# Performance work log

Hardware: AMD Instinct MI355X
Metric: run time of the kernel (lower is better)

The kernel has to match this reference:

```python
import jax, jax.numpy as jnp
import numpy as np

LAMBDA = 0.0   # lambda_value
EPS = 1e-8     # eps


def setup_inputs() -> dict:
    key = jax.random.key(0)
    k1, k2 = jax.random.split(key)
    B, T, C = 512, 256, 400
    outputs = jax.random.normal(k1, (B, T, C), dtype=jnp.float32)
    labels = jax.random.randint(k2, (B,), 0, C, dtype=jnp.int64)
    return {"outputs": outputs, "labels": labels}


def reference(outputs, labels):
    # outputs: (B, T, C) logits; labels: (B,) class indices
    B, T, C = outputs.shape
    proba = jnp.maximum(jax.nn.softmax(outputs, axis=-1), EPS)          # (B,T,C)
    idx = jnp.argmax(proba, axis=1)                                      # (B,C) argmax over time
    max_probs = jnp.maximum(jnp.max(proba, axis=1), EPS)                 # (B,C)
    # parallel prefix-max over the time axis (torch.cummax dim=1)
    cum_max = jax.lax.associative_scan(jnp.maximum, proba, axis=1)       # (B,T,C)
    sum_cum_max = jnp.sum(cum_max, axis=1)                               # (B,C)
    e_x = T - sum_cum_max / max_probs                                    # (B,C) expected exit time
    i_x = e_x / T
    log_term = jnp.log(LAMBDA + (1.0 - LAMBDA) * i_x + EPS)              # (B,C)
    per_class = -jnp.log(max_probs) + log_term                           # (B,C)
    fast_loss = jnp.take_along_axis(per_class, labels[:, None], axis=1)[:, 0]  # (B,)
    fast_loss = fast_loss.mean()                                         # reduction='mean'
    return fast_loss, idx, max_probs, e_x
```

## Files before the change

### kernel.cpp

```cpp
#include <hip/hip_runtime.h>
#include <math.h>

#define B_DIM 512
#define T_DIM 256
#define C_DIM 400
#define EPSV 1e-8f
#define TT 16
#define NT (T_DIM / TT)
#define TILE_F (TT * C_DIM)


__device__ __forceinline__ void load_tile_rows(
    const float* __restrict__ xb, int tile, int w, int ln,
    float4& a0, float4& a1, float4& b0, float4& b1) {
    const float4* r0 = (const float4*)(xb + (size_t)tile * TILE_F + (size_t)(2 * w) * C_DIM);
    const float4* r1 = (const float4*)(xb + (size_t)tile * TILE_F + (size_t)(2 * w + 1) * C_DIM);
    a0 = r0[ln];
    b0 = r1[ln];
    a1 = make_float4(-INFINITY, -INFINITY, -INFINITY, -INFINITY);
    b1 = a1;
    if (ln < 36) { a1 = r0[64 + ln]; b1 = r1[64 + ln]; }
}

__device__ __forceinline__ float wave_sum_dpp(float v) {
    int t;
    t = __builtin_amdgcn_update_dpp(0, __float_as_int(v), 0x111, 0xf, 0xf, true);
    v += __int_as_float(t);
    t = __builtin_amdgcn_update_dpp(0, __float_as_int(v), 0x112, 0xf, 0xf, true);
    v += __int_as_float(t);
    t = __builtin_amdgcn_update_dpp(0, __float_as_int(v), 0x114, 0xf, 0xf, true);
    v += __int_as_float(t);
    t = __builtin_amdgcn_update_dpp(0, __float_as_int(v), 0x118, 0xf, 0xf, true);
    v += __int_as_float(t);
    t = __builtin_amdgcn_update_dpp(0, __float_as_int(v), 0x142, 0xa, 0xf, true);
    v += __int_as_float(t);
    t = __builtin_amdgcn_update_dpp(0, __float_as_int(v), 0x143, 0xc, 0xf, true);
    v += __int_as_float(t);
    return __int_as_float(__builtin_amdgcn_readlane(__float_as_int(v), 63));
}

__device__ __forceinline__ void row_softmax_store(
    float4 v0, float4 v1, float* __restrict__ rowp, int ln) {
    float e0x = __expf(v0.x), e0y = __expf(v0.y);
    float e0z = __expf(v0.z), e0w = __expf(v0.w);
    float e1x = __expf(v1.x), e1y = __expf(v1.y);
    float e1z = __expf(v1.z), e1w = __expf(v1.w);

    float s = wave_sum_dpp(((e0x + e0y) + (e0z + e0w)) +
                           ((e1x + e1y) + (e1z + e1w)));
    float rinv = 1.0f / s;
    float4* wp = (float4*)rowp;
    wp[ln] = make_float4(e0x * rinv, e0y * rinv, e0z * rinv, e0w * rinv);
    if (ln < 36)
        wp[64 + ln] = make_float4(e1x * rinv, e1y * rinv, e1z * rinv, e1w * rinv);
}

__global__ __launch_bounds__(512, 4) void fused_kernel(
    const float* __restrict__ x, const int* __restrict__ labels,
    float* __restrict__ out, double* __restrict__ pcws) {
    __shared__ __align__(16) float buf[2][TILE_F];

    const int b   = blockIdx.x;
    const int tid = threadIdx.x;
    const int w   = tid >> 6;
    const int ln  = tid & 63;
    const int c   = w * 50 + ln;
    const bool act = (ln < 50);
    const float* xb = x + (size_t)b * T_DIM * C_DIM;

    float4 ca0, ca1, cb0, cb1, na0, na1, nb0, nb1;
    load_tile_rows(xb, 0, w, ln, ca0, ca1, cb0, cb1);

    float  cur = EPSV;
    int    arg = 0;
    double scm = 0.0;

    for (int tile = 0; tile < NT; ++tile) {
        const int pb = tile & 1;
        if (tile + 1 < NT)
            load_tile_rows(xb, tile + 1, w, ln, na0, na1, nb0, nb1);

        row_softmax_store(ca0, ca1, &buf[pb][(size_t)(2 * w) * C_DIM], ln);
        row_softmax_store(cb0, cb1, &buf[pb][(size_t)(2 * w + 1) * C_DIM], ln);

        asm volatile("s_waitcnt lgkmcnt(0)" ::: "memory");
        __builtin_amdgcn_sched_barrier(0);
        __builtin_amdgcn_s_barrier();

        if (act) {
            const float* bp = &buf[pb][c];
            float scmt = 0.0f;
            #pragma unroll
            for (int t = 0; t < TT; ++t) {
                float p = bp[(size_t)t * C_DIM];
                if (p > cur) { cur = p; arg = tile * TT + t; }
                scmt += cur;
            }
            scm += (double)scmt;
        }
        ca0 = na0; ca1 = na1; cb0 = nb0; cb1 = nb1;
    }

    if (act) {
        float  maxp = cur;
        double e_x  = (double)T_DIM - scm / (double)maxp;
        if (e_x < 0.0) e_x = 0.0;
        size_t BC = (size_t)B_DIM * C_DIM;
        size_t o  = (size_t)b * C_DIM + c;
        out[1 + o]          = (float)arg;
        out[1 + BC + o]     = maxp;
        out[1 + 2 * BC + o] = (float)e_x;
        if (c == labels[b]) {
            double i_x = e_x / (double)T_DIM;
            pcws[b] = -log((double)maxp) + log(i_x + 1e-8);
        }
    }
}

__global__ __launch_bounds__(512) void loss_kernel(
    const double* __restrict__ pcws, float* __restrict__ out) {
    __shared__ double part[8];
    double pc = pcws[threadIdx.x];
    #pragma unroll
    for (int off = 32; off > 0; off >>= 1)
        pc += __shfl_xor(pc, off, 64);
    if ((threadIdx.x & 63) == 0) part[threadIdx.x >> 6] = pc;
    __syncthreads();
    if (threadIdx.x == 0) {
        double s = 0.0;
        #pragma unroll
        for (int i = 0; i < 8; ++i) s += part[i];
        out[0] = (float)(s / (double)B_DIM);
    }
}

extern "C" void kernel_launch(void* const* d_in, const int* in_sizes, int n_in,
                              void* d_out, int out_size, void* d_ws, size_t ws_size,
                              hipStream_t stream) {
    const float* x      = (const float*)d_in[0];
    const int*   labels = (const int*)d_in[1];
    float*       out    = (float*)d_out;
    double*      pcws   = (double*)d_ws;

    fused_kernel<<<B_DIM, 512, 0, stream>>>(x, labels, out, pcws);
    loss_kernel<<<1, 512, 0, stream>>>(pcws, out);
}
```

Baseline: 40.34 us.

## Pack two batch rows per 1024-thread block with ping-pong softmax/scan phases

Each block now handles two batch rows. The two 512-thread halves alternate each step: one half writes softmax rows to its shared buffer while the other half scans its buffer for running max and argmax, so exp work and LDS scan work interleave across a shared barrier. Each half now uses a single buffer instead of double buffering. Both halves still sync on every barrier, which doubles the barrier count and halves the number of blocks. The reciprocal also changes to the fast hardware rcp, which may shift precision slightly.

```diff
diff --git a/kernel.cpp b/kernel.cpp
--- a/kernel.cpp
+++ b/kernel.cpp
@@ -48,25 +48,28 @@
 
     float s = wave_sum_dpp(((e0x + e0y) + (e0z + e0w)) +
                            ((e1x + e1y) + (e1z + e1w)));
-    float rinv = 1.0f / s;
+    float rinv = __builtin_amdgcn_rcpf(s);
     float4* wp = (float4*)rowp;
     wp[ln] = make_float4(e0x * rinv, e0y * rinv, e0z * rinv, e0w * rinv);
     if (ln < 36)
         wp[64 + ln] = make_float4(e1x * rinv, e1y * rinv, e1z * rinv, e1w * rinv);
 }
 
-__global__ __launch_bounds__(512, 4) void fused_kernel(
+__global__ __launch_bounds__(1024, 4) void fused_kernel(
     const float* __restrict__ x, const int* __restrict__ labels,
     float* __restrict__ out, double* __restrict__ pcws) {
     __shared__ __align__(16) float buf[2][TILE_F];
 
-    const int b   = blockIdx.x;
-    const int tid = threadIdx.x;
-    const int w   = tid >> 6;
-    const int ln  = tid & 63;
-    const int c   = w * 50 + ln;
+    const int tid  = threadIdx.x;
+    const int half = tid >> 9;
+    const int htid = tid & 511;
+    const int w    = htid >> 6;
+    const int ln   = tid & 63;
+    const int b    = blockIdx.x * 2 + half;
+    const int c    = w * 50 + ln;
     const bool act = (ln < 50);
     const float* xb = x + (size_t)b * T_DIM * C_DIM;
+    float* mybuf = &buf[half][0];
 
     float4 ca0, ca1, cb0, cb1, na0, na1, nb0, nb1;
     load_tile_rows(xb, 0, w, ln, ca0, ca1, cb0, cb1);
@@ -75,30 +78,34 @@
     int    arg = 0;
     double scm = 0.0;
 
-    for (int tile = 0; tile < NT; ++tile) {
-        const int pb = tile & 1;
-        if (tile + 1 < NT)
-            load_tile_rows(xb, tile + 1, w, ln, na0, na1, nb0, nb1);
-
-        row_softmax_store(ca0, ca1, &buf[pb][(size_t)(2 * w) * C_DIM], ln);
-        row_softmax_store(cb0, cb1, &buf[pb][(size_t)(2 * w + 1) * C_DIM], ln);
-
+    for (int k = 0; k <= 2 * NT; ++k) {
+        const bool do_stats = ((k & 1) == half);
+        if (do_stats) {
+            const int st = (k - half) >> 1;
+            if (st < NT) {
+                if (st + 1 < NT)
+                    load_tile_rows(xb, st + 1, w, ln, na0, na1, nb0, nb1);
+                row_softmax_store(ca0, ca1, mybuf + (size_t)(2 * w) * C_DIM, ln);
+                row_softmax_store(cb0, cb1, mybuf + (size_t)(2 * w + 1) * C_DIM, ln);
+                ca0 = na0; ca1 = na1; cb0 = nb0; cb1 = nb1;
+            }
+        } else {
+            const int sc = (k - 1 - half) >> 1;
+            if (sc >= 0 && act) {
+                const float* bp = mybuf + c;
+                float scmt = 0.0f;
+                #pragma unroll
+                for (int t = 0; t < TT; ++t) {
+                    float p = bp[(size_t)t * C_DIM];
+                    if (p > cur) { cur = p; arg = sc * TT + t; }
+                    scmt += cur;
+                }
+                scm += (double)scmt;
+            }
+        }
         asm volatile("s_waitcnt lgkmcnt(0)" ::: "memory");
         __builtin_amdgcn_sched_barrier(0);
         __builtin_amdgcn_s_barrier();
-
-        if (act) {
-            const float* bp = &buf[pb][c];
-            float scmt = 0.0f;
-            #pragma unroll
-            for (int t = 0; t < TT; ++t) {
-                float p = bp[(size_t)t * C_DIM];
-                if (p > cur) { cur = p; arg = tile * TT + t; }
-                scmt += cur;
-            }
-            scm += (double)scmt;
-        }
-        ca0 = na0; ca1 = na1; cb0 = nb0; cb1 = nb1;
     }
 
     if (act) {
@@ -142,6 +149,6 @@
     float*       out    = (float*)d_out;
     double*      pcws   = (double*)d_ws;
 
-    fused_kernel<<<B_DIM, 512, 0, stream>>>(x, labels, out, pcws);
+    fused_kernel<<<B_DIM / 2, 1024, 0, stream>>>(x, labels, out, pcws);
     loss_kernel<<<1, 512, 0, stream>>>(pcws, out);
 }
```

After: 45.97 us. +13.9%, slower.

## Software-pipeline softmax stores with scan of previous tile, unroll by two

Applied to the files above, without the earlier changes.

Restructures the tile loop so that the softmax computation and LDS store of the next tile happen in the same barrier phase as the cumulative-max scan of the previous tile. Two named register sets replace the register copies, and the loop is manually unrolled by two with #pragma unroll 1. This lets the exp and row-reduction work overlap with the LDS reads of the scan and drops the register moves. It also swaps the division for a hardware reciprocal, which may differ slightly in precision. The two barriers per pair of tiles stay the same, and register pressure rises from holding two prefetched tiles.

```diff
diff --git a/kernel.cpp b/kernel.cpp
--- a/kernel.cpp
+++ b/kernel.cpp
@@ -48,7 +48,7 @@
 
     float s = wave_sum_dpp(((e0x + e0y) + (e0z + e0w)) +
                            ((e1x + e1y) + (e1z + e1w)));
-    float rinv = 1.0f / s;
+    float rinv = __builtin_amdgcn_rcpf(s);
     float4* wp = (float4*)rowp;
     wp[ln] = make_float4(e0x * rinv, e0y * rinv, e0z * rinv, e0w * rinv);
     if (ln < 36)
@@ -68,37 +68,62 @@
     const bool act = (ln < 50);
     const float* xb = x + (size_t)b * T_DIM * C_DIM;
 
-    float4 ca0, ca1, cb0, cb1, na0, na1, nb0, nb1;
-    load_tile_rows(xb, 0, w, ln, ca0, ca1, cb0, cb1);
+    float4 Aa0, Aa1, Ab0, Ab1;
+    float4 Ba0, Ba1, Bb0, Bb1;
 
     float  cur = EPSV;
     int    arg = 0;
     double scm = 0.0;
 
-    for (int tile = 0; tile < NT; ++tile) {
-        const int pb = tile & 1;
-        if (tile + 1 < NT)
-            load_tile_rows(xb, tile + 1, w, ln, na0, na1, nb0, nb1);
+    load_tile_rows(xb, 0, w, ln, Aa0, Aa1, Ab0, Ab1);
+    load_tile_rows(xb, 1, w, ln, Ba0, Ba1, Bb0, Bb1);
+    row_softmax_store(Aa0, Aa1, &buf[0][(size_t)(2 * w) * C_DIM], ln);
+    row_softmax_store(Ab0, Ab1, &buf[0][(size_t)(2 * w + 1) * C_DIM], ln);
+    asm volatile("s_waitcnt lgkmcnt(0)" ::: "memory");
+    __builtin_amdgcn_sched_barrier(0);
+    __builtin_amdgcn_s_barrier();
 
-        row_softmax_store(ca0, ca1, &buf[pb][(size_t)(2 * w) * C_DIM], ln);
-        row_softmax_store(cb0, cb1, &buf[pb][(size_t)(2 * w + 1) * C_DIM], ln);
-
+    #pragma unroll 1
+    for (int i = 0; i < NT; i += 2) {
+        if (i + 2 < NT)
+            load_tile_rows(xb, i + 2, w, ln, Aa0, Aa1, Ab0, Ab1);
+        row_softmax_store(Ba0, Ba1, &buf[1][(size_t)(2 * w) * C_DIM], ln);
+        row_softmax_store(Bb0, Bb1, &buf[1][(size_t)(2 * w + 1) * C_DIM], ln);
+        if (act) {
+            const float* bp = &buf[0][c];
+            float scmt = 0.0f;
+            #pragma unroll
+            for (int t = 0; t < TT; ++t) {
+                float p = bp[(size_t)t * C_DIM];
+                if (p > cur) { cur = p; arg = i * TT + t; }
+                scmt += cur;
+            }
+            scm += (double)scmt;
+        }
         asm volatile("s_waitcnt lgkmcnt(0)" ::: "memory");
         __builtin_amdgcn_sched_barrier(0);
         __builtin_amdgcn_s_barrier();
 
+        if (i + 3 < NT)
+            load_tile_rows(xb, i + 3, w, ln, Ba0, Ba1, Bb0, Bb1);
+        if (i + 2 < NT) {
+            row_softmax_store(Aa0, Aa1, &buf[0][(size_t)(2 * w) * C_DIM], ln);
+            row_softmax_store(Ab0, Ab1, &buf[0][(size_t)(2 * w + 1) * C_DIM], ln);
+        }
         if (act) {
-            const float* bp = &buf[pb][c];
+            const float* bp = &buf[1][c];
             float scmt = 0.0f;
             #pragma unroll
             for (int t = 0; t < TT; ++t) {
                 float p = bp[(size_t)t * C_DIM];
-                if (p > cur) { cur = p; arg = tile * TT + t; }
+                if (p > cur) { cur = p; arg = (i + 1) * TT + t; }
                 scmt += cur;
             }
             scm += (double)scmt;
         }
-        ca0 = na0; ca1 = na1; cb0 = nb0; cb1 = nb1;
+        asm volatile("s_waitcnt lgkmcnt(0)" ::: "memory");
+        __builtin_amdgcn_sched_barrier(0);
+        __builtin_amdgcn_s_barrier();
     }
 
     if (act) {
```

Result: no change. 40.63 us (+0.7%).
